# Optimization experiments

Hardware: AMD Instinct MI355X
Metric: run time of the kernel (lower is better)

## Reference

```python
import jax, jax.numpy as jnp
import numpy as np

B, H, W, C = 2, 96, 192, 768
NH, HD = 12, 64
W0, W1 = 8, 8          # window size
S0, S1 = 4, 4          # shift size
N = W0 * W1
NW = (H // W0) * (W // W1)
HID = 3072             # mlp_ratio 4 * dim
SCALE = HD ** -0.5


def _ln(x, g, b):
    m = x.mean(-1, keepdims=True)
    v = ((x - m) ** 2).mean(-1, keepdims=True)
    return (x - m) * jax.lax.rsqrt(v + 1e-5) * g + b


def _partition(x):  # (B,H,W,C) -> (B*NW, W0, W1, C)
    Bb = x.shape[0]
    x = x.reshape(Bb, H // W0, W0, W // W1, W1, -1).transpose(0, 1, 3, 2, 4, 5)
    return x.reshape(-1, W0, W1, x.shape[-1])


def _reverse(w):  # (B*NW, W0, W1, C) -> (B,H,W,C)
    Cc = w.shape[-1]
    x = w.reshape(B, H // W0, W // W1, W0, W1, Cc).transpose(0, 1, 3, 2, 4, 5)
    return x.reshape(B, H, W, Cc)


def _rope2(x):  # axial 2D RoPE on (nB, W0, W1, HD): first half rotates over h, second over w
    dh = HD // 2

    def cs(L, d):
        inv = 1.0 / (10000.0 ** (jnp.arange(0, d, 2, dtype=jnp.float32) / d))
        ang = jnp.arange(L, dtype=jnp.float32)[:, None] * inv
        return jnp.cos(ang), jnp.sin(ang)

    def rot(xa, cos, sin):
        x1, x2 = xa[..., 0::2], xa[..., 1::2]
        return jnp.stack([x1 * cos - x2 * sin, x1 * sin + x2 * cos], -1).reshape(xa.shape)

    ch, sh = cs(W0, dh)
    cw, sw = cs(W1, dh)
    xh = rot(x[..., :dh], ch[:, None, :], sh[:, None, :])
    xw = rot(x[..., dh:], cw[None, :, :], sw[None, :, :])
    return jnp.concatenate([xh, xw], -1)


def _make_mask():
    # faithful port of BasicLayer.create_mask (2D path)
    img = np.zeros((H, W), np.float32)
    cnt = 0
    for hs in (slice(0, -W0), slice(-W0, -S0), slice(-S0, None)):
        for wsl in (slice(0, -W1), slice(-W1, 0), slice(0, None)):
            img[hs, wsl] = cnt
            cnt += 1
    mw = img.reshape(H // W0, W0, W // W1, W1).transpose(0, 2, 1, 3).reshape(NW, N)
    am = mw[:, None, :] - mw[:, :, None]
    return jnp.asarray(np.where(am != 0, -100.0, 0.0).astype(np.float32))


def setup_inputs():
    key = jax.random.key(0)
    ks = jax.random.split(key, 6)
    s = lambda k, shape, fan: jax.random.normal(k, shape, jnp.float32) * (fan ** -0.5)
    return dict(
        x=jax.random.normal(ks[0], (B, H * W, C), jnp.float32),
        mask=_make_mask(),
        w_qkv=s(ks[1], (3 * C, C), C), b_qkv=jnp.zeros((3 * C,), jnp.float32),
        w_proj=s(ks[2], (C, C), C), b_proj=jnp.zeros((C,), jnp.float32),
        g1=jnp.ones((C,), jnp.float32), b1=jnp.zeros((C,), jnp.float32),
        g2=jnp.ones((C,), jnp.float32), b2=jnp.zeros((C,), jnp.float32),
        w_fc1=s(ks[3], (HID, C), C), b_fc1=jnp.zeros((HID,), jnp.float32),
        w_fc2=s(ks[4], (C, HID), HID), b_fc2=jnp.zeros((C,), jnp.float32),
    )


def reference(x, mask, w_qkv, b_qkv, w_proj, b_proj, g1, b1, g2, b2,
              w_fc1, b_fc1, w_fc2, b_fc2):
    shortcut = x
    xi = x.reshape(B, H, W, C)
    xi = jnp.roll(xi, (-S0, -S1), axis=(1, 2))
    xw = _partition(xi).reshape(-1, N, C)  # (B*NW, N, C)
    B_ = xw.shape[0]
    qkv = (xw @ w_qkv.T + b_qkv).reshape(B_, N, 3, NH, HD).transpose(2, 0, 3, 1, 4)
    q, k, v = qkv[0], qkv[1], qkv[2]  # (B_, NH, N, HD)
    q = _rope2(q.reshape(-1, W0, W1, HD)).reshape(B_, NH, N, HD)
    k = _rope2(k.reshape(-1, W0, W1, HD)).reshape(B_, NH, N, HD)
    attn = jnp.einsum('bhnd,bhmd->bhnm', q * SCALE, k)
    attn = attn.reshape(B, NW, NH, N, N) + mask[None, :, None]
    attn = jax.nn.softmax(attn.reshape(B_, NH, N, N), axis=-1)
    out = jnp.einsum('bhnm,bhmd->bnhd', attn, v).reshape(B_, N, C)
    out = out @ w_proj.T + b_proj
    xr = _reverse(out.reshape(-1, W0, W1, C))
    xr = jnp.roll(xr, (S0, S1), axis=(1, 2)).reshape(B, H * W, C)
    x1 = _ln(shortcut + xr, g1, b1)          # post-norm residual, as in source
    h = jax.nn.relu(x1 @ w_fc1.T + b_fc1) @ w_fc2.T + b_fc2
    return _ln(x1 + h, g2, b2)
```

## Files before the change

kernel.cpp:

```cpp
#include <hip/hip_runtime.h>
#include <math.h>
#include <stddef.h>

#define NTOK   36864
#define CDIM   768
#define HIDDIM 3072
#define QKVDIM 2304

typedef unsigned short u16;
typedef unsigned int   u32;
typedef __attribute__((ext_vector_type(8))) short short8;
typedef __attribute__((ext_vector_type(4))) short short4v;
typedef __attribute__((ext_vector_type(4))) float f32x4;

__device__ __forceinline__ float bf2f(u16 h) { return __uint_as_float(((u32)h) << 16); }
__device__ __forceinline__ u16 f2bf(float f) {
  u32 u = __float_as_uint(f);
  u32 r = u + 0x7fffu + ((u >> 16) & 1u);
  return (u16)(r >> 16);
}

__device__ __forceinline__ int win_row_to_src(int r) {
  int n = r & 63;
  int wflat = r >> 6;
  int b = wflat / 288;
  int wi = wflat - b * 288;
  int wh = wi / 24;
  int ww = wi - wh * 24;
  int i0 = n >> 3, i1 = n & 7;
  int hh = wh * 8 + i0 + 4; if (hh >= 96)  hh -= 96;
  int wp = ww * 8 + i1 + 4; if (wp >= 192) wp -= 192;
  return b * 18432 + hh * 192 + wp;
}

__device__ __forceinline__ void load_lds16(const u16* g, u16* l) {
  __builtin_amdgcn_global_load_lds((const __attribute__((address_space(1))) void*)g,
                                   (__attribute__((address_space(3))) void*)l, 16, 0, 0);
}

template<int OUTBF, int RELU, int RES>
__launch_bounds__(512, 4)
__global__ void gemm128(const u16* __restrict__ A, const u16* __restrict__ Wt,
                        const float* __restrict__ bias, const u16* __restrict__ res,
                        void* __restrict__ Cout, int M, int N, int K,
                        int gridx, int nwg)
{
  const int orig = blockIdx.x;
  const int xcd  = orig & 7;
  const int q    = nwg >> 3, r8 = nwg & 7;
  const int wgid = (xcd < r8 ? xcd * (q + 1) : r8 * (q + 1) + (xcd - r8) * q) + (orig >> 3);
  int bn, bm;
  if (((gridx | nwg) & 1) == 0) {
    const int halfn = nwg >> 1, hc = gridx >> 1;
    const int half  = (wgid >= halfn) ? 1 : 0;
    const int w2    = wgid - half * halfn;
    bn = (w2 % hc + half * hc) * 128;
    bm = (w2 / hc) * 128;
  } else {
    bn = (wgid % gridx) * 128;
    bm = (wgid / gridx) * 128;
  }

  __shared__ __align__(16) u16 lds[2][2][128 * 64];

  const int t    = threadIdx.x;
  const int wv   = t >> 6, lane = t & 63;
  const int wm   = wv >> 2, wn = wv & 3;
  const int lr   = lane & 15, lg = lane >> 4;
  const int sr   = t >> 3;
  const int ss   = t & 7;

  const u16* Abase = A  + (size_t)bm * K;
  const u16* Bbase = Wt + (size_t)bn * K;

  const int nt = K >> 6;

  auto stage = [&](int kt, int b) {
    const int k0 = kt << 6;
#pragma unroll
    for (int j = 0; j < 2; j++) {
      int row  = j * 64 + sr;
      int slot = ss ^ (row & 7);
      load_lds16(Abase + (size_t)row * K + k0 + slot * 8, &lds[b][0][j * 4096 + t * 8]);
    }
#pragma unroll
    for (int j = 0; j < 2; j++) {
      int row  = j * 64 + sr;
      int slot = ss ^ (row & 7);
      load_lds16(Bbase + (size_t)row * K + k0 + slot * 8, &lds[b][1][j * 4096 + t * 8]);
    }
  };

  f32x4 acc[4][2] = {};

  stage(0, 0);
  stage(1, 1);

  for (int tt = 0; tt < nt; tt++) {
    const int cur = tt & 1;
    if (tt + 1 < nt) asm volatile("s_waitcnt vmcnt(4)" ::: "memory");
    else             asm volatile("s_waitcnt vmcnt(0)" ::: "memory");
    __builtin_amdgcn_s_barrier();

    const u16* Ab = &lds[cur][0][0];
    const u16* Bb = &lds[cur][1][0];

    short8 bfr[2][2], afr[2][2];
#pragma unroll
    for (int nf = 0; nf < 2; nf++)
#pragma unroll
      for (int ks = 0; ks < 2; ks++) {
        int row = wn * 32 + nf * 16 + lr;
        bfr[nf][ks] = *(const short8*)(Bb + row * 64 + (((ks * 4 + lg) ^ (row & 7)) << 3));
      }
#pragma unroll
    for (int mf = 0; mf < 2; mf++)
#pragma unroll
      for (int ks = 0; ks < 2; ks++) {
        int row = wm * 64 + mf * 16 + lr;
        afr[mf][ks] = *(const short8*)(Ab + row * 64 + (((ks * 4 + lg) ^ (row & 7)) << 3));
      }
    asm volatile("s_waitcnt lgkmcnt(0)" ::: "memory");
    __builtin_amdgcn_sched_barrier(0);
    __builtin_amdgcn_s_setprio(1);
#pragma unroll
    for (int ks = 0; ks < 2; ks++)
#pragma unroll
      for (int mf = 0; mf < 2; mf++)
#pragma unroll
        for (int nf = 0; nf < 2; nf++)
          acc[mf][nf] = __builtin_amdgcn_mfma_f32_16x16x32_bf16(bfr[nf][ks], afr[mf][ks], acc[mf][nf], 0, 0, 0);
    __builtin_amdgcn_s_setprio(0);

    short8 afr2[2][2];
#pragma unroll
    for (int mf = 0; mf < 2; mf++)
#pragma unroll
      for (int ks = 0; ks < 2; ks++) {
        int row = wm * 64 + (mf + 2) * 16 + lr;
        afr2[mf][ks] = *(const short8*)(Ab + row * 64 + (((ks * 4 + lg) ^ (row & 7)) << 3));
      }
    asm volatile("s_waitcnt lgkmcnt(0)" ::: "memory");
    __builtin_amdgcn_sched_barrier(0);
    __builtin_amdgcn_s_barrier();

    if (tt + 2 < nt) stage(tt + 2, cur);

    __builtin_amdgcn_s_setprio(1);
#pragma unroll
    for (int ks = 0; ks < 2; ks++)
#pragma unroll
      for (int mf = 0; mf < 2; mf++)
#pragma unroll
        for (int nf = 0; nf < 2; nf++)
          acc[mf + 2][nf] = __builtin_amdgcn_mfma_f32_16x16x32_bf16(bfr[nf][ks], afr2[mf][ks], acc[mf + 2][nf], 0, 0, 0);
    __builtin_amdgcn_s_setprio(0);
  }

#pragma unroll
  for (int mf = 0; mf < 4; mf++) {
    size_t row = (size_t)(bm + wm * 64 + mf * 16 + lr);
#pragma unroll
    for (int nf = 0; nf < 2; nf++) {
      int col0 = bn + wn * 32 + nf * 16 + lg * 4;
      float4 b4 = *(const float4*)(bias + col0);
      float v0 = acc[mf][nf][0] + b4.x;
      float v1 = acc[mf][nf][1] + b4.y;
      float v2 = acc[mf][nf][2] + b4.z;
      float v3 = acc[mf][nf][3] + b4.w;
      if (RELU) {
        v0 = fmaxf(v0, 0.f); v1 = fmaxf(v1, 0.f);
        v2 = fmaxf(v2, 0.f); v3 = fmaxf(v3, 0.f);
      }
      if (RES) {
        short4v rv = *(const short4v*)(res + row * N + col0);
        v0 += bf2f((u16)rv[0]); v1 += bf2f((u16)rv[1]);
        v2 += bf2f((u16)rv[2]); v3 += bf2f((u16)rv[3]);
      }
      if (OUTBF) {
        short4v o;
        o[0] = (short)f2bf(v0); o[1] = (short)f2bf(v1);
        o[2] = (short)f2bf(v2); o[3] = (short)f2bf(v3);
        *(short4v*)((u16*)Cout + row * N + col0) = o;
      } else {
        f32x4 o = {v0, v1, v2, v3};
        *(f32x4*)((float*)Cout + row * N + col0) = o;
      }
    }
  }
}

__launch_bounds__(256)
__global__ void gather_x_bf16(const float* __restrict__ x, u16* __restrict__ xg)
{
  const int t = threadIdx.x, wv = t >> 6, lane = t & 63;
  const int r = blockIdx.x * 4 + wv;
  const float4* src = (const float4*)(x + (size_t)win_row_to_src(r) * CDIM);
  short4v* dst = (short4v*)(xg + (size_t)r * CDIM);
#pragma unroll
  for (int e = 0; e < 3; e++) {
    float4 f = src[e * 64 + lane];
    short4v o;
    o[0] = (short)f2bf(f.x); o[1] = (short)f2bf(f.y);
    o[2] = (short)f2bf(f.z); o[3] = (short)f2bf(f.w);
    dst[e * 64 + lane] = o;
  }
}

__launch_bounds__(256)
__global__ void conv_bf16(const float* __restrict__ in, u16* __restrict__ out, int n)
{
  int i = blockIdx.x * 256 + threadIdx.x;
  if (i < n) out[i] = f2bf(in[i]);
}

__launch_bounds__(256)
__global__ void attn_mfma(const u16* __restrict__ qkv, const float* __restrict__ mask,
                          u16* __restrict__ out)
{
  __shared__ u16 vt[4][4096];
  __shared__ u16 pbuf[4][4096];
  __shared__ float ropetab[512];

  const int t = threadIdx.x;
  {
    int p = t >> 3, pos = t & 7;
    float inv = __expf(-(float)(p & 15) * 0.5756462732485115f);
    float sv, cv;
    sincosf((float)pos * inv, &sv, &cv);
    ropetab[t * 2]     = cv;
    ropetab[t * 2 + 1] = sv;
  }
  __syncthreads();

  const int wv = t >> 6, lane = t & 63;
  const int lr = lane & 15, lg = lane >> 4;
  const int gp   = blockIdx.x * 4 + wv;
  const int head = gp % 12;
  const int lw   = gp / 12;
  const int widx = lw % 288;
  const u16* base = qkv + (size_t)lw * 64 * QKVDIM + head * 64;

  {
    const u16* vrow = base + 1536 + (size_t)lane * QKVDIM;
    u16* vb = vt[wv];
#pragma unroll
    for (int s = 0; s < 8; s++) {
      short8 v = *(const short8*)(vrow + s * 8);
#pragma unroll
      for (int j = 0; j < 8; j++) {
        int d = s * 8 + j;
        vb[d * 64 + ((((lane >> 3) ^ (d & 7)) << 3) | (lane & 7))] = (u16)v[j];
      }
    }
  }

  short8 aq[4][2], ak[4][2];
#pragma unroll
  for (int f = 0; f < 4; f++) {
#pragma unroll
    for (int ks = 0; ks < 2; ks++) {
      int n = f * 16 + lr;
      short8 qv = *(const short8*)(base + (size_t)n * QKVDIM + ks * 32 + lg * 8);
      short8 kv = *(const short8*)(base + (size_t)n * QKVDIM + 768 + ks * 32 + lg * 8);
      short8 qo, ko;
#pragma unroll
      for (int jj = 0; jj < 4; jj++) {
        int p   = ks * 16 + lg * 4 + jj;
        int pos = (p < 16) ? (n >> 3) : (n & 7);
        float cv = ropetab[(p * 8 + pos) * 2];
        float sv = ropetab[(p * 8 + pos) * 2 + 1];
        float q1 = bf2f((u16)qv[2 * jj]), q2 = bf2f((u16)qv[2 * jj + 1]);
        float k1 = bf2f((u16)kv[2 * jj]), k2 = bf2f((u16)kv[2 * jj + 1]);
        qo[2 * jj]     = (short)f2bf((q1 * cv - q2 * sv) * 0.125f);
        qo[2 * jj + 1] = (short)f2bf((q1 * sv + q2 * cv) * 0.125f);
        ko[2 * jj]     = (short)f2bf(k1 * cv - k2 * sv);
        ko[2 * jj + 1] = (short)f2bf(k1 * sv + k2 * cv);
      }
      aq[f][ks] = qo; ak[f][ks] = ko;
    }
  }

  f32x4 sf[4][4] = {};
#pragma unroll
  for (int ks = 0; ks < 2; ks++)
#pragma unroll
    for (int fn = 0; fn < 4; fn++)
#pragma unroll
      for (int fm = 0; fm < 4; fm++)
        sf[fn][fm] = __builtin_amdgcn_mfma_f32_16x16x32_bf16(aq[fn][ks], ak[fm][ks], sf[fn][fm], 0, 0, 0);

  const float* mrow = mask + (size_t)widx * 4096;
#pragma unroll
  for (int fn = 0; fn < 4; fn++)
#pragma unroll
    for (int fm = 0; fm < 4; fm++)
#pragma unroll
      for (int j = 0; j < 4; j++)
        sf[fn][fm][j] += mrow[(fn * 16 + lg * 4 + j) * 64 + fm * 16 + lr];

#pragma unroll
  for (int fn = 0; fn < 4; fn++) {
#pragma unroll
    for (int j = 0; j < 4; j++) {
      float m0 = fmaxf(fmaxf(sf[fn][0][j], sf[fn][1][j]),
                       fmaxf(sf[fn][2][j], sf[fn][3][j]));
      m0 = fmaxf(m0, __shfl_xor(m0, 1));
      m0 = fmaxf(m0, __shfl_xor(m0, 2));
      m0 = fmaxf(m0, __shfl_xor(m0, 4));
      m0 = fmaxf(m0, __shfl_xor(m0, 8));
      float s0 = 0.f;
#pragma unroll
      for (int fm = 0; fm < 4; fm++) {
        float e = __expf(sf[fn][fm][j] - m0);
        sf[fn][fm][j] = e;
        s0 += e;
      }
      s0 += __shfl_xor(s0, 1);
      s0 += __shfl_xor(s0, 2);
      s0 += __shfl_xor(s0, 4);
      s0 += __shfl_xor(s0, 8);
      float r = 1.f / s0;
#pragma unroll
      for (int fm = 0; fm < 4; fm++) sf[fn][fm][j] *= r;
    }
  }

  u16* pb = pbuf[wv];
#pragma unroll
  for (int fn = 0; fn < 4; fn++)
#pragma unroll
    for (int fm = 0; fm < 4; fm++)
#pragma unroll
      for (int j = 0; j < 4; j++) {
        int n = fn * 16 + lg * 4 + j, m = fm * 16 + lr;
        pb[n * 64 + ((((m >> 3) ^ (n & 7)) << 3) | (m & 7))] = f2bf(sf[fn][fm][j]);
      }
  asm volatile("s_waitcnt lgkmcnt(0)" ::: "memory");
  __builtin_amdgcn_sched_barrier(0);

  short8 ap[4][2], bvf[4][2];
#pragma unroll
  for (int f = 0; f < 4; f++)
#pragma unroll
    for (int ks = 0; ks < 2; ks++) {
      int rn = f * 16 + lr;
      ap[f][ks]  = *(const short8*)(pb     + rn * 64 + (((ks * 4 + lg) ^ (rn & 7)) << 3));
      bvf[f][ks] = *(const short8*)(vt[wv] + rn * 64 + (((ks * 4 + lg) ^ (rn & 7)) << 3));
    }
  f32x4 o[4][4] = {};
#pragma unroll
  for (int ks = 0; ks < 2; ks++)
#pragma unroll
    for (int fn = 0; fn < 4; fn++)
#pragma unroll
      for (int fd = 0; fd < 4; fd++)
        o[fn][fd] = __builtin_amdgcn_mfma_f32_16x16x32_bf16(bvf[fd][ks], ap[fn][ks], o[fn][fd], 0, 0, 0);

  u16* ob = out + ((size_t)lw * 64) * CDIM + head * 64;
#pragma unroll
  for (int fn = 0; fn < 4; fn++) {
    size_t nrow = (size_t)(fn * 16 + lr) * CDIM;
#pragma unroll
    for (int fd = 0; fd < 4; fd++) {
      int d0 = fd * 16 + lg * 4;
      short4v ov;
      ov[0] = (short)f2bf(o[fn][fd][0]);
      ov[1] = (short)f2bf(o[fn][fd][1]);
      ov[2] = (short)f2bf(o[fn][fd][2]);
      ov[3] = (short)f2bf(o[fn][fd][3]);
      *(short4v*)(ob + nrow + d0) = ov;
    }
  }
}

__launch_bounds__(256)
__global__ void ln1_kernel(const u16* __restrict__ xg, const u16* __restrict__ add,
                           const float* __restrict__ g, const float* __restrict__ bb,
                           u16* __restrict__ out)
{
  const int t = threadIdx.x, wv = t >> 6, lane = t & 63;
  const int tok = blockIdx.x * 4 + wv;
  int b = tok / 18432;
  int hw = tok - b * 18432;
  int h = hw / 192, w = hw - h * 192;
  int h2 = h - 4; if (h2 < 0) h2 += 96;
  int w2 = w - 4; if (w2 < 0) w2 += 192;
  int r = ((b * 12 + (h2 >> 3)) * 24 + (w2 >> 3)) * 64 + (h2 & 7) * 8 + (w2 & 7);
  const short4v* a0 = (const short4v*)(xg  + (size_t)r * CDIM);
  const short4v* a1 = (const short4v*)(add + (size_t)r * CDIM);

  float v[12];
  float s1 = 0.f, s2 = 0.f;
#pragma unroll
  for (int e = 0; e < 3; e++) {
    short4v f = a0[e * 64 + lane];
    short4v a = a1[e * 64 + lane];
#pragma unroll
    for (int j = 0; j < 4; j++) {
      float x = bf2f((u16)f[j]) + bf2f((u16)a[j]);
      v[e*4+j] = x; s1 += x; s2 += x * x;
    }
  }
#pragma unroll
  for (int m = 1; m < 64; m <<= 1) {
    s1 += __shfl_xor(s1, m);
    s2 += __shfl_xor(s2, m);
  }
  float mean = s1 * (1.f / 768.f);
  float var  = s2 * (1.f / 768.f) - mean * mean;
  float rs   = rsqrtf(var + 1e-5f);
  short4v* dst = (short4v*)(out + (size_t)tok * CDIM);
#pragma unroll
  for (int e = 0; e < 3; e++) {
    short4v o;
#pragma unroll
    for (int j = 0; j < 4; j++) {
      int c = (e * 64 + lane) * 4 + j;
      o[j] = (short)f2bf((v[e*4+j] - mean) * rs * g[c] + bb[c]);
    }
    dst[e * 64 + lane] = o;
  }
}

__launch_bounds__(256)
__global__ void ln2_kernel(const u16* __restrict__ xin, const float* __restrict__ g,
                           const float* __restrict__ bb, float* __restrict__ out)
{
  const int t = threadIdx.x, wv = t >> 6, lane = t & 63;
  const int tok = blockIdx.x * 4 + wv;
  const short4v* a0 = (const short4v*)(xin + (size_t)tok * CDIM);

  float v[12];
  float s1 = 0.f, s2 = 0.f;
#pragma unroll
  for (int e = 0; e < 3; e++) {
    short4v a = a0[e * 64 + lane];
#pragma unroll
    for (int j = 0; j < 4; j++) {
      float x = bf2f((u16)a[j]);
      v[e*4+j] = x; s1 += x; s2 += x * x;
    }
  }
#pragma unroll
  for (int m = 1; m < 64; m <<= 1) {
    s1 += __shfl_xor(s1, m);
    s2 += __shfl_xor(s2, m);
  }
  float mean = s1 * (1.f / 768.f);
  float var  = s2 * (1.f / 768.f) - mean * mean;
  float rs   = rsqrtf(var + 1e-5f);
  float4* dst = (float4*)(out + (size_t)tok * CDIM);
#pragma unroll
  for (int e = 0; e < 3; e++) {
    float4 o;
    int c = (e * 64 + lane) * 4;
    o.x = (v[e*4+0] - mean) * rs * g[c+0] + bb[c+0];
    o.y = (v[e*4+1] - mean) * rs * g[c+1] + bb[c+1];
    o.z = (v[e*4+2] - mean) * rs * g[c+2] + bb[c+2];
    o.w = (v[e*4+3] - mean) * rs * g[c+3] + bb[c+3];
    dst[e * 64 + lane] = o;
  }
}

static inline void launch_gemm(const u16* A, const u16* Wt, const float* bias,
                               const u16* res, void* C, int M, int N, int K,
                               int outbf, int relu, int resf, hipStream_t s)
{
  int gridx = N / 128, nwg = gridx * (M / 128);
  if (outbf) {
    if (relu)      gemm128<1,1,0><<<nwg, 512, 0, s>>>(A, Wt, bias, res, C, M, N, K, gridx, nwg);
    else if (resf) gemm128<1,0,1><<<nwg, 512, 0, s>>>(A, Wt, bias, res, C, M, N, K, gridx, nwg);
    else           gemm128<1,0,0><<<nwg, 512, 0, s>>>(A, Wt, bias, res, C, M, N, K, gridx, nwg);
  } else {
    gemm128<0,0,0><<<nwg, 512, 0, s>>>(A, Wt, bias, res, C, M, N, K, gridx, nwg);
  }
}

extern "C" void kernel_launch(void* const* d_in, const int* in_sizes, int n_in,
                              void* d_out, int out_size, void* d_ws, size_t ws_size,
                              hipStream_t stream)
{
  const float* x      = (const float*)d_in[0];
  const float* mask   = (const float*)d_in[1];
  const float* w_qkv  = (const float*)d_in[2];
  const float* b_qkv  = (const float*)d_in[3];
  const float* w_proj = (const float*)d_in[4];
  const float* b_proj = (const float*)d_in[5];
  const float* g1     = (const float*)d_in[6];
  const float* b1     = (const float*)d_in[7];
  const float* g2     = (const float*)d_in[8];
  const float* b2     = (const float*)d_in[9];
  const float* w_fc1  = (const float*)d_in[10];
  const float* b_fc1  = (const float*)d_in[11];
  const float* w_fc2  = (const float*)d_in[12];
  const float* b_fc2  = (const float*)d_in[13];
  float* out = (float*)d_out;

  char* base = (char*)d_ws;
  u16* A0 = (u16*)base;
  u16* A1 = (u16*)(base + 56623104);
  u16* A2 = (u16*)(base + 226492416);
  u16* Hb = (u16*)base;
  u16* wqkvb  = (u16*)(base + 283115520);
  u16* wprojb = wqkvb  + 1769472;
  u16* wfc1b  = wprojb + 589824;
  u16* wfc2b  = wfc1b  + 2359296;

  conv_bf16<<<(1769472 + 255) / 256, 256, 0, stream>>>(w_qkv,  wqkvb,  1769472);
  conv_bf16<<<( 589824 + 255) / 256, 256, 0, stream>>>(w_proj, wprojb,  589824);
  conv_bf16<<<(2359296 + 255) / 256, 256, 0, stream>>>(w_fc1,  wfc1b,  2359296);
  conv_bf16<<<(2359296 + 255) / 256, 256, 0, stream>>>(w_fc2,  wfc2b,  2359296);
  gather_x_bf16<<<NTOK / 4, 256, 0, stream>>>(x, A0);

  launch_gemm(A0, wqkvb, b_qkv, nullptr, A1, NTOK, QKVDIM, CDIM, 1, 0, 0, stream);
  attn_mfma<<<576 * 12 / 4, 256, 0, stream>>>(A1, mask, A2);

  launch_gemm(A2, wprojb, b_proj, nullptr, A1, NTOK, CDIM, CDIM, 1, 0, 0, stream);

  ln1_kernel<<<NTOK / 4, 256, 0, stream>>>(A0, A1, g1, b1, A2);

  launch_gemm(A2, wfc1b, b_fc1, nullptr, Hb, NTOK, HIDDIM, CDIM, 1, 1, 0, stream);
  launch_gemm(Hb, wfc2b, b_fc2, A2, A2, NTOK, CDIM, HIDDIM, 1, 0, 1, stream);

  ln2_kernel<<<NTOK / 4, 256, 0, stream>>>(A2, g2, b2, out);
}
```

Baseline: 866.2 us.

## Switch GEMM to 256x128 tiles with 4 waves and K-step 32

Replaces the 128x128 GEMM tile run by 8 waves with a 256x128 tile run by 4 waves. Each wave now computes a 128x64 sub-tile with a 32-wide K slice per stage, which raises MFMA work per LDS fragment load and halves the number of workgroups. The cost is far more accumulator registers per thread (32 f32x4), lower occupancy, twice as many barrier iterations, and fewer workgroups to spread across CUs.

```diff
diff --git a/kernel.cpp b/kernel.cpp
--- a/kernel.cpp
+++ b/kernel.cpp
@@ -39,11 +39,11 @@
 }
 
 template<int OUTBF, int RELU, int RES>
-__launch_bounds__(512, 4)
-__global__ void gemm128(const u16* __restrict__ A, const u16* __restrict__ Wt,
-                        const float* __restrict__ bias, const u16* __restrict__ res,
-                        void* __restrict__ Cout, int M, int N, int K,
-                        int gridx, int nwg)
+__launch_bounds__(256, 2)
+__global__ void gemm256x128(const u16* __restrict__ A, const u16* __restrict__ Wt,
+                            const float* __restrict__ bias, const u16* __restrict__ res,
+                            void* __restrict__ Cout, int M, int N, int K,
+                            int gridx, int nwg)
 {
   const int orig = blockIdx.x;
   const int xcd  = orig & 7;
@@ -55,91 +55,84 @@
     const int half  = (wgid >= halfn) ? 1 : 0;
     const int w2    = wgid - half * halfn;
     bn = (w2 % hc + half * hc) * 128;
-    bm = (w2 / hc) * 128;
+    bm = (w2 / hc) * 256;
   } else {
     bn = (wgid % gridx) * 128;
-    bm = (wgid / gridx) * 128;
-  }
-
-  __shared__ __align__(16) u16 lds[2][2][128 * 64];
+    bm = (wgid / gridx) * 256;
+  }
+
+  __shared__ __align__(16) u16 Asm[2][256 * 32];
+  __shared__ __align__(16) u16 Bsm[2][128 * 32];
 
   const int t    = threadIdx.x;
   const int wv   = t >> 6, lane = t & 63;
-  const int wm   = wv >> 2, wn = wv & 3;
+  const int wm   = wv >> 1, wn = wv & 1;
   const int lr   = lane & 15, lg = lane >> 4;
-  const int sr   = t >> 3;
-  const int ss   = t & 7;
+  const int sr   = t >> 2;
+  const int sc   = t & 3;
 
   const u16* Abase = A  + (size_t)bm * K;
   const u16* Bbase = Wt + (size_t)bn * K;
 
-  const int nt = K >> 6;
+  const int nt = K >> 5;
 
   auto stage = [&](int kt, int b) {
-    const int k0 = kt << 6;
+    const int k0 = kt << 5;
+#pragma unroll
+    for (int j = 0; j < 4; j++) {
+      int row  = j * 64 + sr;
+      int slot = sc ^ (row & 3);
+      load_lds16(Abase + (size_t)row * K + k0 + slot * 8, &Asm[b][j * 2048 + t * 8]);
+    }
 #pragma unroll
     for (int j = 0; j < 2; j++) {
       int row  = j * 64 + sr;
-      int slot = ss ^ (row & 7);
-      load_lds16(Abase + (size_t)row * K + k0 + slot * 8, &lds[b][0][j * 4096 + t * 8]);
-    }
-#pragma unroll
-    for (int j = 0; j < 2; j++) {
-      int row  = j * 64 + sr;
-      int slot = ss ^ (row & 7);
-      load_lds16(Bbase + (size_t)row * K + k0 + slot * 8, &lds[b][1][j * 4096 + t * 8]);
+      int slot = sc ^ (row & 3);
+      load_lds16(Bbase + (size_t)row * K + k0 + slot * 8, &Bsm[b][j * 2048 + t * 8]);
     }
   };
 
-  f32x4 acc[4][2] = {};
+  f32x4 acc[8][4] = {};
 
   stage(0, 0);
   stage(1, 1);
 
   for (int tt = 0; tt < nt; tt++) {
     const int cur = tt & 1;
-    if (tt + 1 < nt) asm volatile("s_waitcnt vmcnt(4)" ::: "memory");
+    if (tt + 1 < nt) asm volatile("s_waitcnt vmcnt(6)" ::: "memory");
     else             asm volatile("s_waitcnt vmcnt(0)" ::: "memory");
     __builtin_amdgcn_s_barrier();
 
-    const u16* Ab = &lds[cur][0][0];
-    const u16* Bb = &lds[cur][1][0];
-
-    short8 bfr[2][2], afr[2][2];
-#pragma unroll
-    for (int nf = 0; nf < 2; nf++)
-#pragma unroll
-      for (int ks = 0; ks < 2; ks++) {
-        int row = wn * 32 + nf * 16 + lr;
-        bfr[nf][ks] = *(const short8*)(Bb + row * 64 + (((ks * 4 + lg) ^ (row & 7)) << 3));
-      }
-#pragma unroll
-    for (int mf = 0; mf < 2; mf++)
-#pragma unroll
-      for (int ks = 0; ks < 2; ks++) {
-        int row = wm * 64 + mf * 16 + lr;
-        afr[mf][ks] = *(const short8*)(Ab + row * 64 + (((ks * 4 + lg) ^ (row & 7)) << 3));
-      }
+    const u16* Ab = &Asm[cur][0];
+    const u16* Bb = &Bsm[cur][0];
+
+    short8 bfr[4], afr[4];
+#pragma unroll
+    for (int nf = 0; nf < 4; nf++) {
+      int row = wn * 64 + nf * 16 + lr;
+      bfr[nf] = *(const short8*)(Bb + row * 32 + ((lg ^ (row & 3)) << 3));
+    }
+#pragma unroll
+    for (int mf = 0; mf < 4; mf++) {
+      int row = wm * 128 + mf * 16 + lr;
+      afr[mf] = *(const short8*)(Ab + row * 32 + ((lg ^ (row & 3)) << 3));
+    }
     asm volatile("s_waitcnt lgkmcnt(0)" ::: "memory");
     __builtin_amdgcn_sched_barrier(0);
     __builtin_amdgcn_s_setprio(1);
 #pragma unroll
-    for (int ks = 0; ks < 2; ks++)
-#pragma unroll
-      for (int mf = 0; mf < 2; mf++)
-#pragma unroll
-        for (int nf = 0; nf < 2; nf++)
-          acc[mf][nf] = __builtin_amdgcn_mfma_f32_16x16x32_bf16(bfr[nf][ks], afr[mf][ks], acc[mf][nf], 0, 0, 0);
+    for (int mf = 0; mf < 4; mf++)
+#pragma unroll
+      for (int nf = 0; nf < 4; nf++)
+        acc[mf][nf] = __builtin_amdgcn_mfma_f32_16x16x32_bf16(bfr[nf], afr[mf], acc[mf][nf], 0, 0, 0);
     __builtin_amdgcn_s_setprio(0);
 
-    short8 afr2[2][2];
-#pragma unroll
-    for (int mf = 0; mf < 2; mf++)
-#pragma unroll
-      for (int ks = 0; ks < 2; ks++) {
-        int row = wm * 64 + (mf + 2) * 16 + lr;
-        afr2[mf][ks] = *(const short8*)(Ab + row * 64 + (((ks * 4 + lg) ^ (row & 7)) << 3));
-      }
+    short8 afr2[4];
+#pragma unroll
+    for (int mf = 0; mf < 4; mf++) {
+      int row = wm * 128 + (mf + 4) * 16 + lr;
+      afr2[mf] = *(const short8*)(Ab + row * 32 + ((lg ^ (row & 3)) << 3));
+    }
     asm volatile("s_waitcnt lgkmcnt(0)" ::: "memory");
     __builtin_amdgcn_sched_barrier(0);
     __builtin_amdgcn_s_barrier();
@@ -148,21 +141,19 @@
 
     __builtin_amdgcn_s_setprio(1);
 #pragma unroll
-    for (int ks = 0; ks < 2; ks++)
-#pragma unroll
-      for (int mf = 0; mf < 2; mf++)
-#pragma unroll
-        for (int nf = 0; nf < 2; nf++)
-          acc[mf + 2][nf] = __builtin_amdgcn_mfma_f32_16x16x32_bf16(bfr[nf][ks], afr2[mf][ks], acc[mf + 2][nf], 0, 0, 0);
+    for (int mf = 0; mf < 4; mf++)
+#pragma unroll
+      for (int nf = 0; nf < 4; nf++)
+        acc[mf + 4][nf] = __builtin_amdgcn_mfma_f32_16x16x32_bf16(bfr[nf], afr2[mf], acc[mf + 4][nf], 0, 0, 0);
     __builtin_amdgcn_s_setprio(0);
   }
 
 #pragma unroll
-  for (int mf = 0; mf < 4; mf++) {
-    size_t row = (size_t)(bm + wm * 64 + mf * 16 + lr);
-#pragma unroll
-    for (int nf = 0; nf < 2; nf++) {
-      int col0 = bn + wn * 32 + nf * 16 + lg * 4;
+  for (int mf = 0; mf < 8; mf++) {
+    size_t row = (size_t)(bm + wm * 128 + mf * 16 + lr);
+#pragma unroll
+    for (int nf = 0; nf < 4; nf++) {
+      int col0 = bn + wn * 64 + nf * 16 + lg * 4;
       float4 b4 = *(const float4*)(bias + col0);
       float v0 = acc[mf][nf][0] + b4.x;
       float v1 = acc[mf][nf][1] + b4.y;
@@ -467,13 +458,13 @@
                                const u16* res, void* C, int M, int N, int K,
                                int outbf, int relu, int resf, hipStream_t s)
 {
-  int gridx = N / 128, nwg = gridx * (M / 128);
+  int gridx = N / 128, nwg = gridx * (M / 256);
   if (outbf) {
-    if (relu)      gemm128<1,1,0><<<nwg, 512, 0, s>>>(A, Wt, bias, res, C, M, N, K, gridx, nwg);
-    else if (resf) gemm128<1,0,1><<<nwg, 512, 0, s>>>(A, Wt, bias, res, C, M, N, K, gridx, nwg);
-    else           gemm128<1,0,0><<<nwg, 512, 0, s>>>(A, Wt, bias, res, C, M, N, K, gridx, nwg);
+    if (relu)      gemm256x128<1,1,0><<<nwg, 256, 0, s>>>(A, Wt, bias, res, C, M, N, K, gridx, nwg);
+    else if (resf) gemm256x128<1,0,1><<<nwg, 256, 0, s>>>(A, Wt, bias, res, C, M, N, K, gridx, nwg);
+    else           gemm256x128<1,0,0><<<nwg, 256, 0, s>>>(A, Wt, bias, res, C, M, N, K, gridx, nwg);
   } else {
-    gemm128<0,0,0><<<nwg, 512, 0, s>>>(A, Wt, bias, res, C, M, N, K, gridx, nwg);
+    gemm256x128<0,0,0><<<nwg, 256, 0, s>>>(A, Wt, bias, res, C, M, N, K, gridx, nwg);
   }
 }
 
```

Result: slower. 910.2 us (+5.1%).
